# Performance work log

Hardware: AMD Instinct MI355X
Metric: run time of the kernel (lower is better)

The kernel has to match this reference:

```python
import jax, jax.numpy as jnp
import numpy as np

N = 50000       # nodes
E = 800000      # edges (before self loops)
F_IN = 256      # num_features
HID = 64        # hidden_dim
HEADS = 4       # num_heads
NEG = 0.2       # negative_slope
LN_EPS = 1e-5


def setup_inputs() -> dict:
    key = jax.random.key(0)
    ks = jax.random.split(key, 24)
    g = lambda k, shape, s=0.05: jax.random.normal(k, shape, jnp.float32) * s
    inp = {
        "x": jax.random.normal(ks[0], (N, F_IN), jnp.float32),
        "edge_index": jax.random.randint(ks[1], (2, E), 0, N, jnp.int32),
        # gat1: in=F_IN, out=HID per head, HEADS heads, concat=True
        "W1": g(ks[2], (HEADS * HID, F_IN)),
        "att_src1": g(ks[3], (HEADS, HID)),
        "att_dst1": g(ks[4], (HEADS, HID)),
        "b1": g(ks[5], (HEADS * HID,)),
        # gat2: in=HEADS*HID, out=HID, 1 head
        "W2": g(ks[6], (HID, HEADS * HID)),
        "att_src2": g(ks[7], (1, HID)),
        "att_dst2": g(ks[8], (1, HID)),
        "b2": g(ks[9], (HID,)),
        # lin_in residual projection
        "lin_w": g(ks[10], (HID, F_IN)),
        "lin_b": g(ks[11], (HID,)),
        # LayerNorm
        "gamma": jnp.ones((HID,), jnp.float32),
        "beta": jnp.zeros((HID,), jnp.float32),
        # GRU (1 layer, input=HID, hidden=HID), gate order r,z,n as in torch
        "w_ih": g(ks[12], (3 * HID, HID)),
        "w_hh": g(ks[13], (3 * HID, HID)),
        "b_ih": g(ks[14], (3 * HID,)),
        "b_hh": g(ks[15], (3 * HID,)),
        # fc head -> 3 classes
        "fc_w": g(ks[16], (3, HID)),
        "fc_b": g(ks[17], (3,)),
    }
    return inp


def gat_conv(x, W, att_src, att_dst, bias, src, dst, heads, n_nodes):
    """PyG-style GATConv (eval mode: no dropout). src/dst include self loops."""
    h = (x @ W.T).reshape(n_nodes, heads, -1)            # [N,H,C]
    a_src = jnp.einsum('nhc,hc->nh', h, att_src)          # [N,H]
    a_dst = jnp.einsum('nhc,hc->nh', h, att_dst)
    e = jax.nn.leaky_relu(a_src[src] + a_dst[dst], NEG)   # [E',H]
    m = jax.ops.segment_max(e, dst, num_segments=n_nodes) # scatter-softmax over dst
    e = jnp.exp(e - m[dst])
    s = jax.ops.segment_sum(e, dst, num_segments=n_nodes)
    alpha = e / s[dst]                                    # [E',H]
    out = jax.ops.segment_sum(alpha[:, :, None] * h[src], dst, num_segments=n_nodes)
    return out.reshape(n_nodes, -1) + bias                # concat heads + bias


def reference(x, edge_index, W1, att_src1, att_dst1, b1, W2, att_src2, att_dst2, b2,
              lin_w, lin_b, gamma, beta, w_ih, w_hh, b_ih, b_hh, fc_w, fc_b):
    n = x.shape[0]
    loops = jnp.arange(n, dtype=edge_index.dtype)
    src = jnp.concatenate([edge_index[0], loops])  # add_self_loops=True default
    dst = jnp.concatenate([edge_index[1], loops])

    h = jax.nn.leaky_relu(gat_conv(x, W1, att_src1, att_dst1, b1, src, dst, HEADS, n), NEG)
    # F.dropout is identity in eval mode
    h = gat_conv(h, W2, att_src2, att_dst2, b2, src, dst, 1, n)
    h = jax.nn.leaky_relu(h, NEG)
    # LayerNorm (torch uses biased variance)
    mu = h.mean(-1, keepdims=True)
    var = ((h - mu) ** 2).mean(-1, keepdims=True)
    h = (h - mu) / jnp.sqrt(var + LN_EPS) * gamma + beta
    h = h + x @ lin_w.T + lin_b
    # single-step GRU with h0 = 0 (seq_len == 1)
    gi = h @ w_ih.T + b_ih                 # [N,3C]
    i_r, i_z, i_n = jnp.split(gi, 3, axis=-1)
    h_r, h_z, h_n = jnp.split(b_hh, 3)     # W_hh @ 0 == 0
    r = jax.nn.sigmoid(i_r + h_r)
    z = jax.nn.sigmoid(i_z + h_z)
    ng = jnp.tanh(i_n + r * h_n)
    hy = (1.0 - z) * ng                    # + z * h_prev(=0)
    return hy @ fc_w.T + fc_b              # [N,3]
```

## Files before the change

### kernel.cpp

```cpp
#include <hip/hip_runtime.h>
#include <hip/hip_bf16.h>

#define N_NODES 50000
#define N_EDGES 800000
#define F_IN 256
#define HID 64
#define HEADS 4
#define NEG 0.2f
#define LN_EPS 1e-5f

typedef _Float16 half8 __attribute__((ext_vector_type(8)));
typedef _Float16 half4v __attribute__((ext_vector_type(4)));
typedef float floatx4 __attribute__((ext_vector_type(4)));

__device__ __forceinline__ float wave_sum(float v) {
    #pragma unroll
    for (int o = 32; o > 0; o >>= 1) v += __shfl_xor(v, o, 64);
    return v;
}
__device__ __forceinline__ int wave_sum_i(int v) {
    #pragma unroll
    for (int o = 32; o > 0; o >>= 1) v += __shfl_xor(v, o, 64);
    return v;
}
__device__ __forceinline__ float leaky(float x) { return x > 0.0f ? x : NEG * x; }

__global__ void count_kernel(const int* __restrict__ dst, int* __restrict__ deg,
                             int E, int Etot) {
    int e = blockIdx.x * blockDim.x + threadIdx.x;
    if (e >= Etot) return;
    int d = (e < E) ? dst[e] : (e - E);
    atomicAdd(&deg[d], 1);
}

__global__ void scan_part(const int* __restrict__ deg, int* __restrict__ bsum, int N) {
    int tid = threadIdx.x;
    int i = blockIdx.x * 256 + tid;
    int v = (i < N) ? deg[i] : 0;
    int s = wave_sum_i(v);
    __shared__ int ws4[4];
    if ((tid & 63) == 0) ws4[tid >> 6] = s;
    __syncthreads();
    if (tid == 0) bsum[blockIdx.x] = ws4[0] + ws4[1] + ws4[2] + ws4[3];
}

__global__ void scan_top(int* __restrict__ bsum, int nb) {
    __shared__ int sh[256];
    int t = threadIdx.x;
    int v = (t < nb) ? bsum[t] : 0;
    sh[t] = v;
    __syncthreads();
    for (int o = 1; o < 256; o <<= 1) {
        int u = (t >= o) ? sh[t - o] : 0;
        __syncthreads();
        sh[t] += u;
        __syncthreads();
    }
    if (t < nb) bsum[t] = sh[t] - v;
}

__global__ void scan_final(const int* __restrict__ deg, const int* __restrict__ bsum,
                           int* __restrict__ row_ptr, int N) {
    __shared__ int sh[256];
    int t = threadIdx.x;
    int i = blockIdx.x * 256 + t;
    int v = (i < N) ? deg[i] : 0;
    sh[t] = v;
    __syncthreads();
    for (int o = 1; o < 256; o <<= 1) {
        int u = (t >= o) ? sh[t - o] : 0;
        __syncthreads();
        sh[t] += u;
        __syncthreads();
    }
    if (i < N) row_ptr[i + 1] = bsum[blockIdx.x] + sh[t];
    if (i == 0) row_ptr[0] = 0;
}

__global__ void scatter_kernel(const int* __restrict__ src, const int* __restrict__ dst,
                               const int* __restrict__ row_ptr, int* __restrict__ fill,
                               int* __restrict__ col, int E, int Etot) {
    int e = blockIdx.x * blockDim.x + threadIdx.x;
    if (e >= Etot) return;
    int s, d;
    if (e < E) { s = src[e]; d = dst[e]; }
    else       { s = d = e - E; }
    int pos = atomicAdd(&fill[d], 1);
    col[row_ptr[d] + pos] = s;
}

struct CvtJob { const float* src; _Float16* dst; int len; };
__global__ void cvt_f16_multi(CvtJob j0, CvtJob j1, CvtJob j2, CvtJob j3, CvtJob j4) {
    int idx = (blockIdx.x * blockDim.x + threadIdx.x) * 4;
    const float* s; _Float16* d; int rel = idx;
    if      (rel < j0.len) { s = j0.src; d = j0.dst; }
    else if ((rel -= j0.len) < j1.len) { s = j1.src; d = j1.dst; }
    else if ((rel -= j1.len) < j2.len) { s = j2.src; d = j2.dst; }
    else if ((rel -= j2.len) < j3.len) { s = j3.src; d = j3.dst; }
    else if ((rel -= j3.len) < j4.len) { s = j4.src; d = j4.dst; }
    else return;
    float4 v = *(const float4*)(s + rel);
    half4v h;
    h[0] = (_Float16)v.x; h[1] = (_Float16)v.y;
    h[2] = (_Float16)v.z; h[3] = (_Float16)v.w;
    *(half4v*)(d + rel) = h;
}

template<int NT, int H, typename OutT>
__global__ __launch_bounds__(256, 2)
void gemm_mfma(const _Float16* __restrict__ A, const _Float16* __restrict__ B,
               const float* __restrict__ bias, OutT* __restrict__ Cout,
               const float* __restrict__ att_s, const float* __restrict__ att_d,
               float* __restrict__ a_srcO, float* __restrict__ a_dstO,
               int M, int K, int add_bias) {
    constexpr int Nc = NT * 16;
    constexpr int BROW = 40;
    constexpr int BTILE = Nc * BROW * 2;
    constexpr int TILEB = 16 * Nc * sizeof(OutT);
    constexpr int SM = (BTILE > 4 * TILEB) ? BTILE : 4 * TILEB;
    __shared__ __align__(16) char smem[SM];
    _Float16* sB = (_Float16*)smem;
    int tid = threadIdx.x;
    int w = tid >> 6, lane = tid & 63;
    int m_base = blockIdx.x * 64 + w * 16;
    bool active = (m_base < M);
    int r = lane & 15, q = lane >> 4;
    const _Float16* ap = A + (size_t)(m_base + r) * K + q * 8;
    floatx4 acc[NT];
    #pragma unroll
    for (int t = 0; t < NT; ++t) acc[t] = (floatx4){0.f, 0.f, 0.f, 0.f};
    half8 a_next = {};
    if (active) a_next = *(const half8*)ap;
    for (int k0 = 0; k0 < K; k0 += 32) {
        for (int i = tid; i < Nc * 4; i += 256) {
            int row = i >> 2, seg = i & 3;
            *(half8*)(sB + row * BROW + seg * 8) =
                *(const half8*)(B + (size_t)row * K + k0 + seg * 8);
        }
        __syncthreads();
        half8 a = a_next;
        if (active && k0 + 32 < K) a_next = *(const half8*)(ap + k0 + 32);
        if (active) {
            half8 b[NT];
            #pragma unroll
            for (int t = 0; t < NT; ++t)
                b[t] = *(const half8*)(sB + (t * 16 + r) * BROW + q * 8);
            #pragma unroll
            for (int t = 0; t < NT; ++t)
                acc[t] = __builtin_amdgcn_mfma_f32_16x16x32_f16(a, b[t], acc[t], 0, 0, 0);
        }
        __syncthreads();
    }
    if (active) {
        OutT* st = (OutT*)(smem + w * TILEB);
        #pragma unroll
        for (int t = 0; t < NT; ++t) {
            int cc = t * 16 + r;
            float bv = add_bias ? bias[cc] : 0.0f;
            #pragma unroll
            for (int rr = 0; rr < 4; ++rr)
                st[(q * 4 + rr) * Nc + cc] = (OutT)(acc[t][rr] + bv);
        }
        constexpr int NISS = TILEB / 1024;
        const int4* src = (const int4*)st;
        int4* dst = (int4*)((char*)Cout + (size_t)m_base * (Nc * sizeof(OutT)));
        #pragma unroll
        for (int i = 0; i < NISS; ++i) dst[i * 64 + lane] = src[i * 64 + lane];
        if constexpr (H > 0) {
            float ps[H][4], pd[H][4];
            #pragma unroll
            for (int h = 0; h < H; ++h) {
                #pragma unroll
                for (int rr = 0; rr < 4; ++rr) { ps[h][rr] = 0.f; pd[h][rr] = 0.f; }
                #pragma unroll
                for (int tt = 0; tt < 4; ++tt) {
                    int t = h * 4 + tt;
                    float as = att_s[t * 16 + r];
                    float ad = att_d[t * 16 + r];
                    #pragma unroll
                    for (int rr = 0; rr < 4; ++rr) {
                        ps[h][rr] += acc[t][rr] * as;
                        pd[h][rr] += acc[t][rr] * ad;
                    }
                }
            }
            #pragma unroll
            for (int m = 1; m < 16; m <<= 1) {
                #pragma unroll
                for (int h = 0; h < H; ++h)
                    #pragma unroll
                    for (int rr = 0; rr < 4; ++rr) {
                        ps[h][rr] += __shfl_xor(ps[h][rr], m, 64);
                        pd[h][rr] += __shfl_xor(pd[h][rr], m, 64);
                    }
            }
            if (r == 0) {
                #pragma unroll
                for (int rr = 0; rr < 4; ++rr) {
                    int gm = m_base + q * 4 + rr;
                    #pragma unroll
                    for (int h = 0; h < H; ++h) {
                        a_srcO[gm * H + h] = ps[h][rr];
                        a_dstO[gm * H + h] = pd[h][rr];
                    }
                }
            }
        }
    }
}

__global__ void gat_agg4(const _Float16* __restrict__ h, const float* __restrict__ a_src,
                         const float* __restrict__ a_dst, const int* __restrict__ row_ptr,
                         const int* __restrict__ col, const float* __restrict__ bias,
                         _Float16* __restrict__ outp, int N) {
    int w = threadIdx.x >> 6, lane = threadIdx.x & 63;
    int i = blockIdx.x * 4 + w;
    if (i >= N) return;
    __shared__ float alphS[4][256];
    __shared__ int   scolS[4][64];
    float* alph = alphS[w];
    int*   scol = scolS[w];
    int start = row_ptr[i], end = row_ptr[i + 1];
    int deg = end - start;
    float4 ad4 = *(const float4*)(a_dst + i * 4);

    if (deg <= 64) {
        float e0 = 0.f, e1 = 0.f, e2 = 0.f, e3 = 0.f; int s = 0;
        if (lane < deg) {
            s = col[start + lane];
            float4 as4 = *(const float4*)(a_src + (size_t)s * 4);
            e0 = __expf(leaky(as4.x + ad4.x));
            e1 = __expf(leaky(as4.y + ad4.y));
            e2 = __expf(leaky(as4.z + ad4.z));
            e3 = __expf(leaky(as4.w + ad4.w));
        }
        float s0 = wave_sum(e0), s1 = wave_sum(e1), s2 = wave_sum(e2), s3 = wave_sum(e3);
        float4 al = make_float4(0.f, 0.f, 0.f, 0.f);
        int so = 0;
        if (lane < deg) {
            al = make_float4(e0 / s0, e1 / s1, e2 / s2, e3 / s3);
            so = s << 9;
        }
        *(float4*)(alph + lane * 4) = al;
        scol[lane] = so;
        int half32 = lane >> 5;
        int fl = lane & 31;
        int flb = fl * 16;
        int ahofs = half32 * 4 + (fl >> 3);
        const char* hB = (const char*)h;
        float acc[8];
        #pragma unroll
        for (int k = 0; k < 8; ++k) acc[k] = 0.f;
        int dpad = (deg + 7) & ~7;
        for (int j = 0; j < dpad; j += 8) {
            int o0 = scol[j + half32];
            int o1 = scol[j + 2 + half32];
            int o2 = scol[j + 4 + half32];
            int o3 = scol[j + 6 + half32];
            half8 v0 = *(const half8*)(hB + (flb + o0));
            half8 v1 = *(const half8*)(hB + (flb + o1));
            half8 v2 = *(const half8*)(hB + (flb + o2));
            half8 v3 = *(const half8*)(hB + (flb + o3));
            float a0 = alph[j * 4 + ahofs];
            float a1 = alph[j * 4 + 8 + ahofs];
            float a2 = alph[j * 4 + 16 + ahofs];
            float a3 = alph[j * 4 + 24 + ahofs];
            #pragma unroll
            for (int k = 0; k < 8; ++k) acc[k] += a0 * (float)v0[k];
            #pragma unroll
            for (int k = 0; k < 8; ++k) acc[k] += a1 * (float)v1[k];
            #pragma unroll
            for (int k = 0; k < 8; ++k) acc[k] += a2 * (float)v2[k];
            #pragma unroll
            for (int k = 0; k < 8; ++k) acc[k] += a3 * (float)v3[k];
        }
        #pragma unroll
        for (int k = 0; k < 8; ++k) acc[k] += __shfl_xor(acc[k], 32, 64);
        if (lane < 32) {
            half8 o8;
            #pragma unroll
            for (int k = 0; k < 8; ++k)
                o8[k] = (_Float16)leaky(acc[k] + bias[fl * 8 + k]);
            *(half8*)(outp + (size_t)i * 256 + fl * 8) = o8;
        }
    } else {
        int hh = lane >> 4;
        const _Float16* hb = h + lane * 4;
        float4 acc = make_float4(0.f, 0.f, 0.f, 0.f);
        float t0 = 0.f, t1 = 0.f, t2 = 0.f, t3 = 0.f;
        for (int j = start + lane; j < end; j += 64) {
            int s = col[j];
            float4 as4 = *(const float4*)(a_src + (size_t)s * 4);
            t0 += __expf(leaky(as4.x + ad4.x));
            t1 += __expf(leaky(as4.y + ad4.y));
            t2 += __expf(leaky(as4.z + ad4.z));
            t3 += __expf(leaky(as4.w + ad4.w));
        }
        t0 = wave_sum(t0); t1 = wave_sum(t1); t2 = wave_sum(t2); t3 = wave_sum(t3);
        float adh = (hh == 0) ? ad4.x : (hh == 1) ? ad4.y : (hh == 2) ? ad4.z : ad4.w;
        float ih  = 1.0f / ((hh == 0) ? t0 : (hh == 1) ? t1 : (hh == 2) ? t2 : t3);
        for (int j = start; j < end; ++j) {
            int s = col[j];
            float asv = a_src[(size_t)s * 4 + hh];
            float alpha = __expf(leaky(asv + adh)) * ih;
            half4v v = *(const half4v*)(hb + (size_t)s * 256);
            acc.x += alpha * (float)v[0]; acc.y += alpha * (float)v[1];
            acc.z += alpha * (float)v[2]; acc.w += alpha * (float)v[3];
        }
        float4 bv = *(const float4*)(bias + lane * 4);
        half4v o;
        o[0] = (_Float16)leaky(acc.x + bv.x);
        o[1] = (_Float16)leaky(acc.y + bv.y);
        o[2] = (_Float16)leaky(acc.z + bv.z);
        o[3] = (_Float16)leaky(acc.w + bv.w);
        *(half4v*)(outp + (size_t)i * 256 + lane * 4) = o;
    }
}

__global__ void gat_agg1_ln(const _Float16* __restrict__ h, const float* __restrict__ a_src,
                            const float* __restrict__ a_dst, const int* __restrict__ row_ptr,
                            const int* __restrict__ col, const float* __restrict__ bias,
                            const float* __restrict__ lin, const float* __restrict__ gamma,
                            const float* __restrict__ beta, _Float16* __restrict__ hresh,
                            int N) {
    int w = threadIdx.x >> 6, lane = threadIdx.x & 63;
    int i = blockIdx.x * 4 + w;
    if (i >= N) return;
    __shared__ float alphS[4][64];
    __shared__ int   scolS[4][64];
    float* alph = alphS[w];
    int*   scol = scolS[w];
    int start = row_ptr[i], end = row_ptr[i + 1];
    int deg = end - start;
    float ad = a_dst[i];
    int sub = lane >> 4;
    int c4 = (lane & 15) * 4;
    float4 acc = make_float4(0.f, 0.f, 0.f, 0.f);

    if (deg <= 64) {
        float e = 0.f; int s = 0;
        if (lane < deg) {
            s = col[start + lane];
            e = __expf(leaky(a_src[s] + ad));
        }
        float ss = wave_sum(e);
        if (lane < deg) { alph[lane] = e / ss; scol[lane] = s; }
        int j = sub;
        for (; j + 4 < deg; j += 8) {
            int s0 = scol[j], s1 = scol[j + 4];
            float a0 = alph[j], a1 = alph[j + 4];
            half4v v0 = *(const half4v*)(h + (size_t)s0 * 64 + c4);
            half4v v1 = *(const half4v*)(h + (size_t)s1 * 64 + c4);
            acc.x += a0 * (float)v0[0] + a1 * (float)v1[0];
            acc.y += a0 * (float)v0[1] + a1 * (float)v1[1];
            acc.z += a0 * (float)v0[2] + a1 * (float)v1[2];
            acc.w += a0 * (float)v0[3] + a1 * (float)v1[3];
        }
        for (; j < deg; j += 4) {
            int s = scol[j];
            float a0 = alph[j];
            half4v v = *(const half4v*)(h + (size_t)s * 64 + c4);
            acc.x += a0 * (float)v[0]; acc.y += a0 * (float)v[1];
            acc.z += a0 * (float)v[2]; acc.w += a0 * (float)v[3];
        }
    } else {
        float ssum = 0.f;
        for (int j = start + lane; j < end; j += 64)
            ssum += __expf(leaky(a_src[col[j]] + ad));
        ssum = wave_sum(ssum);
        float inv = 1.0f / ssum;
        for (int j = start + sub; j < end; j += 4) {
            int s = col[j];
            float alpha = __expf(leaky(a_src[s] + ad)) * inv;
            half4v v = *(const half4v*)(h + (size_t)s * 64 + c4);
            acc.x += alpha * (float)v[0]; acc.y += alpha * (float)v[1];
            acc.z += alpha * (float)v[2]; acc.w += alpha * (float)v[3];
        }
    }
    #pragma unroll
    for (int o = 16; o <= 32; o <<= 1) {
        acc.x += __shfl_xor(acc.x, o, 64);
        acc.y += __shfl_xor(acc.y, o, 64);
        acc.z += __shfl_xor(acc.z, o, 64);
        acc.w += __shfl_xor(acc.w, o, 64);
    }
    float4 bv = *(const float4*)(bias + c4);
    float o0 = leaky(acc.x + bv.x), o1 = leaky(acc.y + bv.y);
    float o2 = leaky(acc.z + bv.z), o3 = leaky(acc.w + bv.w);
    float ls = o0 + o1 + o2 + o3;
    #pragma unroll
    for (int o = 1; o <= 8; o <<= 1) ls += __shfl_xor(ls, o, 64);
    float mu = ls * (1.0f / 64.0f);
    float d0 = o0 - mu, d1 = o1 - mu, d2 = o2 - mu, d3 = o3 - mu;
    float lq = d0 * d0 + d1 * d1 + d2 * d2 + d3 * d3;
    #pragma unroll
    for (int o = 1; o <= 8; o <<= 1) lq += __shfl_xor(lq, o, 64);
    float rstd = rsqrtf(lq * (1.0f / 64.0f) + LN_EPS);
    float4 g4 = *(const float4*)(gamma + c4);
    float4 b4 = *(const float4*)(beta + c4);
    float4 l4 = *(const float4*)(lin + (size_t)i * 64 + c4);
    if (sub == 0) {
        half4v hv;
        hv[0] = (_Float16)(d0 * rstd * g4.x + b4.x + l4.x);
        hv[1] = (_Float16)(d1 * rstd * g4.y + b4.y + l4.y);
        hv[2] = (_Float16)(d2 * rstd * g4.z + b4.z + l4.z);
        hv[3] = (_Float16)(d3 * rstd * g4.w + b4.w + l4.w);
        *(half4v*)(hresh + (size_t)i * 64 + c4) = hv;
    }
}

__global__ __launch_bounds__(256, 2)
void gemm_gru(const _Float16* __restrict__ A, const _Float16* __restrict__ B,
              const float* __restrict__ b_ih, const float* __restrict__ b_hh,
              const float* __restrict__ fc_w, const float* __restrict__ fc_b,
              float* __restrict__ outp, int M) {
    const int K = 64, NT = 12, Nc = 192;
    constexpr int BROW = 40;
    __shared__ __align__(16) char smem[4 * 16 * 192 * 2];
    _Float16* sB = (_Float16*)smem;
    int tid = threadIdx.x;
    int w = tid >> 6, lane = tid & 63;
    int m_base = blockIdx.x * 64 + w * 16;
    bool active = (m_base < M);
    int r = lane & 15, q = lane >> 4;
    const _Float16* ap = A + (size_t)(m_base + r) * K + q * 8;
    floatx4 acc[NT];
    #pragma unroll
    for (int t = 0; t < NT; ++t) acc[t] = (floatx4){0.f, 0.f, 0.f, 0.f};
    half8 a_next = {};
    if (active) a_next = *(const half8*)ap;
    for (int k0 = 0; k0 < K; k0 += 32) {
        for (int i = tid; i < Nc * 4; i += 256) {
            int row = i >> 2, seg = i & 3;
            *(half8*)(sB + row * BROW + seg * 8) =
                *(const half8*)(B + (size_t)row * K + k0 + seg * 8);
        }
        __syncthreads();
        half8 a = a_next;
        if (active && k0 + 32 < K) a_next = *(const half8*)(ap + k0 + 32);
        if (active) {
            half8 b[NT];
            #pragma unroll
            for (int t = 0; t < NT; ++t)
                b[t] = *(const half8*)(sB + (t * 16 + r) * BROW + q * 8);
            #pragma unroll
            for (int t = 0; t < NT; ++t)
                acc[t] = __builtin_amdgcn_mfma_f32_16x16x32_f16(a, b[t], acc[t], 0, 0, 0);
        }
        __syncthreads();
    }
    if (!active) return;
    _Float16* sw = (_Float16*)smem + w * 16 * 192;
    #pragma unroll
    for (int t = 0; t < NT; ++t) {
        int cc = t * 16 + r;
        float bv = b_ih[cc];
        #pragma unroll
        for (int rr = 0; rr < 4; ++rr)
            sw[(q * 4 + rr) * Nc + cc] = (_Float16)(acc[t][rr] + bv);
    }
    float br_[4], bz_[4], bn_[4], f0_[4], f1_[4], f2_[4];
    *(float4*)br_ = *(const float4*)(b_hh + r * 4);
    *(float4*)bz_ = *(const float4*)(b_hh + 64 + r * 4);
    *(float4*)bn_ = *(const float4*)(b_hh + 128 + r * 4);
    *(float4*)f0_ = *(const float4*)(fc_w + r * 4);
    *(float4*)f1_ = *(const float4*)(fc_w + 64 + r * 4);
    *(float4*)f2_ = *(const float4*)(fc_w + 128 + r * 4);
    #pragma unroll
    for (int rr = 0; rr < 4; ++rr) {
        int row = q * 4 + rr;
        const _Float16* g = sw + row * Nc;
        half4v ir4 = *(const half4v*)(g + r * 4);
        half4v iz4 = *(const half4v*)(g + 64 + r * 4);
        half4v in4 = *(const half4v*)(g + 128 + r * 4);
        float p0 = 0.f, p1 = 0.f, p2 = 0.f;
        #pragma unroll
        for (int k = 0; k < 4; ++k) {
            float rg = 1.0f / (1.0f + __expf(-((float)ir4[k] + br_[k])));
            float zg = 1.0f / (1.0f + __expf(-((float)iz4[k] + bz_[k])));
            float ng = tanhf((float)in4[k] + rg * bn_[k]);
            float hy = (1.0f - zg) * ng;
            p0 += hy * f0_[k]; p1 += hy * f1_[k]; p2 += hy * f2_[k];
        }
        #pragma unroll
        for (int o = 1; o <= 8; o <<= 1) {
            p0 += __shfl_xor(p0, o, 64);
            p1 += __shfl_xor(p1, o, 64);
            p2 += __shfl_xor(p2, o, 64);
        }
        if (r == 0) {
            int gm = m_base + row;
            outp[(size_t)gm * 3 + 0] = p0 + fc_b[0];
            outp[(size_t)gm * 3 + 1] = p1 + fc_b[1];
            outp[(size_t)gm * 3 + 2] = p2 + fc_b[2];
        }
    }
}

extern "C" void kernel_launch(void* const* d_in, const int* in_sizes, int n_in,
                              void* d_out, int out_size, void* d_ws, size_t ws_size,
                              hipStream_t stream) {
    const float* x        = (const float*)d_in[0];
    const int*   ei       = (const int*)d_in[1];
    const float* W1       = (const float*)d_in[2];
    const float* att_src1 = (const float*)d_in[3];
    const float* att_dst1 = (const float*)d_in[4];
    const float* b1       = (const float*)d_in[5];
    const float* W2       = (const float*)d_in[6];
    const float* att_src2 = (const float*)d_in[7];
    const float* att_dst2 = (const float*)d_in[8];
    const float* b2       = (const float*)d_in[9];
    const float* lin_w    = (const float*)d_in[10];
    const float* lin_b    = (const float*)d_in[11];
    const float* gamma    = (const float*)d_in[12];
    const float* beta     = (const float*)d_in[13];
    const float* w_ih     = (const float*)d_in[14];
    const float* b_ih     = (const float*)d_in[16];
    const float* b_hh     = (const float*)d_in[17];
    const float* fc_w     = (const float*)d_in[18];
    const float* fc_b     = (const float*)d_in[19];
    float* out = (float*)d_out;

    const int N = N_NODES, E = N_EDGES;
    const int Etot = E + N;
    const int nb = (N + 255) / 256;
    char* ws = (char*)d_ws;

    size_t off = 0;
    auto alloc = [&](size_t bytes) {
        size_t o = off;
        off = (off + bytes + 255) & ~(size_t)255;
        return o;
    };
    int*      row_ptr = (int*)(ws + alloc((size_t)(N + 1) * 4));
    int*      col     = (int*)(ws + alloc((size_t)Etot * 4));
    int*      deg     = (int*)(ws + alloc((size_t)N * 4));
    int*      fill    = (int*)(ws + alloc((size_t)N * 4));
    int*      bsum    = (int*)(ws + alloc((size_t)nb * 4));
    float*    a_src1b = (float*)(ws + alloc((size_t)N * HEADS * 4));
    float*    a_dst1b = (float*)(ws + alloc((size_t)N * HEADS * 4));
    float*    a_src2b = (float*)(ws + alloc((size_t)N * 4));
    float*    a_dst2b = (float*)(ws + alloc((size_t)N * 4));
    _Float16* W1h     = (_Float16*)(ws + alloc((size_t)256 * 256 * 2));
    _Float16* W2h     = (_Float16*)(ws + alloc((size_t)64 * 256 * 2));
    _Float16* lin_wh  = (_Float16*)(ws + alloc((size_t)64 * 256 * 2));
    _Float16* w_ihh   = (_Float16*)(ws + alloc((size_t)192 * 64 * 2));
    char* big = ws + alloc((size_t)64000000);
    _Float16* xh   = (_Float16*)big;
    _Float16* h1h  = (_Float16*)(big + 25600000);
    float*    lin  = (float*)(big + 51200000);
    char* r3 = ws + alloc((size_t)25600000);
    _Float16* o1h   = (_Float16*)r3;
    _Float16* hresh = (_Float16*)r3;
    char* r4 = ws + alloc((size_t)6400000);
    _Float16* h2h = (_Float16*)r4;

    hipMemsetAsync(deg, 0, (size_t)N * 4, stream);
    hipMemsetAsync(fill, 0, (size_t)N * 4, stream);

    count_kernel<<<(Etot + 255) / 256, 256, 0, stream>>>(ei + E, deg, E, Etot);
    scan_part<<<nb, 256, 0, stream>>>(deg, bsum, N);
    scan_top<<<1, 256, 0, stream>>>(bsum, nb);
    scan_final<<<nb, 256, 0, stream>>>(deg, bsum, row_ptr, N);
    scatter_kernel<<<(Etot + 255) / 256, 256, 0, stream>>>(ei, ei + E, row_ptr, fill, col, E, Etot);

    {
        CvtJob j0{x, xh, N * F_IN};
        CvtJob j1{W1, W1h, 256 * 256};
        CvtJob j2{W2, W2h, 64 * 256};
        CvtJob j3{lin_w, lin_wh, 64 * 256};
        CvtJob j4{w_ih, w_ihh, 192 * 64};
        int total4 = (j0.len + j1.len + j2.len + j3.len + j4.len) / 4;
        cvt_f16_multi<<<(total4 + 255) / 256, 256, 0, stream>>>(j0, j1, j2, j3, j4);
    }

    const int gmBlocks = (N + 63) / 64;
    const int aggBlocks = (N + 3) / 4;

    gemm_mfma<16, 4, _Float16><<<gmBlocks, 256, 0, stream>>>(xh, W1h, nullptr, h1h,
        att_src1, att_dst1, a_src1b, a_dst1b, N, 256, 0);
    gat_agg4<<<aggBlocks, 256, 0, stream>>>(h1h, a_src1b, a_dst1b, row_ptr, col, b1, o1h, N);

    gemm_mfma<4, 0, float><<<gmBlocks, 256, 0, stream>>>(xh, lin_wh, lin_b, lin,
        nullptr, nullptr, nullptr, nullptr, N, 256, 1);

    gemm_mfma<4, 1, _Float16><<<gmBlocks, 256, 0, stream>>>(o1h, W2h, nullptr, h2h,
        att_src2, att_dst2, a_src2b, a_dst2b, N, 256, 0);

    gat_agg1_ln<<<aggBlocks, 256, 0, stream>>>(h2h, a_src2b, a_dst2b, row_ptr, col, b2,
        lin, gamma, beta, hresh, N);

    gemm_gru<<<gmBlocks, 256, 0, stream>>>(hresh, w_ihh, b_ih, b_hh, fc_w, fc_b, out, N);
}
```

Baseline: 371.8 us.

## Fuse lin_in projection into layer-1 GEMM and use packed fp16 FMA in aggregation

The residual lin_in projection is merged into the first GAT GEMM by concatenating its weights after W1, giving a 320-column fp16 output whose last 64 columns hold the residual. This removes a separate GEMM launch and its second read of x, and the residual is now stored in fp16 instead of fp32. The layer-1 aggregation also switches to packed half2 FMAs with fp16 attention weights, partially accumulating in fp16 before adding into fp32. The cost is a wider row stride (640 bytes) for gathers, and some precision loss from fp16 alpha, fp16 partial sums and the fp16 residual.

```diff
diff --git a/kernel.cpp b/kernel.cpp
--- a/kernel.cpp
+++ b/kernel.cpp
@@ -11,7 +11,11 @@
 
 typedef _Float16 half8 __attribute__((ext_vector_type(8)));
 typedef _Float16 half4v __attribute__((ext_vector_type(4)));
+typedef _Float16 half2v __attribute__((ext_vector_type(2)));
 typedef float floatx4 __attribute__((ext_vector_type(4)));
+
+union H2U { unsigned u; half2v h; };
+union H8U { half8 v; half2v h2[4]; };
 
 __device__ __forceinline__ float wave_sum(float v) {
     #pragma unroll
@@ -112,7 +116,7 @@
                const float* __restrict__ bias, OutT* __restrict__ Cout,
                const float* __restrict__ att_s, const float* __restrict__ att_d,
                float* __restrict__ a_srcO, float* __restrict__ a_dstO,
-               int M, int K, int add_bias) {
+               int M, int K, int bias_mode) {
     constexpr int Nc = NT * 16;
     constexpr int BROW = 40;
     constexpr int BTILE = Nc * BROW * 2;
@@ -156,7 +160,9 @@
         #pragma unroll
         for (int t = 0; t < NT; ++t) {
             int cc = t * 16 + r;
-            float bv = add_bias ? bias[cc] : 0.0f;
+            float bv = 0.f;
+            if (bias_mode == 1) bv = bias[cc];
+            else if (bias_mode == 2 && cc >= 256) bv = bias[cc - 256];
             #pragma unroll
             for (int rr = 0; rr < 4; ++rr)
                 st[(q * 4 + rr) * Nc + cc] = (OutT)(acc[t][rr] + bv);
@@ -216,10 +222,10 @@
     int w = threadIdx.x >> 6, lane = threadIdx.x & 63;
     int i = blockIdx.x * 4 + w;
     if (i >= N) return;
-    __shared__ float alphS[4][256];
-    __shared__ int   scolS[4][64];
-    float* alph = alphS[w];
-    int*   scol = scolS[w];
+    __shared__ unsigned alphS[4][256];
+    __shared__ int      scolS[4][64];
+    unsigned* alph = alphS[w];
+    int*      scol = scolS[w];
     int start = row_ptr[i], end = row_ptr[i + 1];
     int deg = end - start;
     float4 ad4 = *(const float4*)(a_dst + i * 4);
@@ -239,9 +245,14 @@
         int so = 0;
         if (lane < deg) {
             al = make_float4(e0 / s0, e1 / s1, e2 / s2, e3 / s3);
-            so = s << 9;
-        }
-        *(float4*)(alph + lane * 4) = al;
+            so = s * 640;
+        }
+        H2U p0, p1, p2, p3;
+        _Float16 t0 = (_Float16)al.x; p0.h = (half2v){t0, t0};
+        _Float16 t1 = (_Float16)al.y; p1.h = (half2v){t1, t1};
+        _Float16 t2 = (_Float16)al.z; p2.h = (half2v){t2, t2};
+        _Float16 t3 = (_Float16)al.w; p3.h = (half2v){t3, t3};
+        *(uint4*)(alph + lane * 4) = make_uint4(p0.u, p1.u, p2.u, p3.u);
         scol[lane] = so;
         int half32 = lane >> 5;
         int fl = lane & 31;
@@ -257,22 +268,25 @@
             int o1 = scol[j + 2 + half32];
             int o2 = scol[j + 4 + half32];
             int o3 = scol[j + 6 + half32];
-            half8 v0 = *(const half8*)(hB + (flb + o0));
-            half8 v1 = *(const half8*)(hB + (flb + o1));
-            half8 v2 = *(const half8*)(hB + (flb + o2));
-            half8 v3 = *(const half8*)(hB + (flb + o3));
-            float a0 = alph[j * 4 + ahofs];
-            float a1 = alph[j * 4 + 8 + ahofs];
-            float a2 = alph[j * 4 + 16 + ahofs];
-            float a3 = alph[j * 4 + 24 + ahofs];
-            #pragma unroll
-            for (int k = 0; k < 8; ++k) acc[k] += a0 * (float)v0[k];
-            #pragma unroll
-            for (int k = 0; k < 8; ++k) acc[k] += a1 * (float)v1[k];
-            #pragma unroll
-            for (int k = 0; k < 8; ++k) acc[k] += a2 * (float)v2[k];
-            #pragma unroll
-            for (int k = 0; k < 8; ++k) acc[k] += a3 * (float)v3[k];
+            H8U v0, v1, v2, v3;
+            v0.v = *(const half8*)(hB + (flb + o0));
+            v1.v = *(const half8*)(hB + (flb + o1));
+            v2.v = *(const half8*)(hB + (flb + o2));
+            v3.v = *(const half8*)(hB + (flb + o3));
+            H2U a0, a1, a2, a3;
+            a0.u = alph[j * 4 + ahofs];
+            a1.u = alph[j * 4 + 8 + ahofs];
+            a2.u = alph[j * 4 + 16 + ahofs];
+            a3.u = alph[j * 4 + 24 + ahofs];
+            #pragma unroll
+            for (int p = 0; p < 4; ++p) {
+                half2v hp = a0.h * v0.h2[p];
+                hp = __builtin_elementwise_fma(a1.h, v1.h2[p], hp);
+                hp = __builtin_elementwise_fma(a2.h, v2.h2[p], hp);
+                hp = __builtin_elementwise_fma(a3.h, v3.h2[p], hp);
+                acc[p * 2]     += (float)hp[0];
+                acc[p * 2 + 1] += (float)hp[1];
+            }
         }
         #pragma unroll
         for (int k = 0; k < 8; ++k) acc[k] += __shfl_xor(acc[k], 32, 64);
@@ -303,7 +317,7 @@
             int s = col[j];
             float asv = a_src[(size_t)s * 4 + hh];
             float alpha = __expf(leaky(asv + adh)) * ih;
-            half4v v = *(const half4v*)(hb + (size_t)s * 256);
+            half4v v = *(const half4v*)(hb + (size_t)s * 320);
             acc.x += alpha * (float)v[0]; acc.y += alpha * (float)v[1];
             acc.z += alpha * (float)v[2]; acc.w += alpha * (float)v[3];
         }
@@ -320,7 +334,7 @@
 __global__ void gat_agg1_ln(const _Float16* __restrict__ h, const float* __restrict__ a_src,
                             const float* __restrict__ a_dst, const int* __restrict__ row_ptr,
                             const int* __restrict__ col, const float* __restrict__ bias,
-                            const float* __restrict__ lin, const float* __restrict__ gamma,
+                            const _Float16* __restrict__ linh, const float* __restrict__ gamma,
                             const float* __restrict__ beta, _Float16* __restrict__ hresh,
                             int N) {
     int w = threadIdx.x >> 6, lane = threadIdx.x & 63;
@@ -398,13 +412,13 @@
     float rstd = rsqrtf(lq * (1.0f / 64.0f) + LN_EPS);
     float4 g4 = *(const float4*)(gamma + c4);
     float4 b4 = *(const float4*)(beta + c4);
-    float4 l4 = *(const float4*)(lin + (size_t)i * 64 + c4);
+    half4v l4 = *(const half4v*)(linh + (size_t)i * 320 + c4);
     if (sub == 0) {
         half4v hv;
-        hv[0] = (_Float16)(d0 * rstd * g4.x + b4.x + l4.x);
-        hv[1] = (_Float16)(d1 * rstd * g4.y + b4.y + l4.y);
-        hv[2] = (_Float16)(d2 * rstd * g4.z + b4.z + l4.z);
-        hv[3] = (_Float16)(d3 * rstd * g4.w + b4.w + l4.w);
+        hv[0] = (_Float16)(d0 * rstd * g4.x + b4.x + (float)l4[0]);
+        hv[1] = (_Float16)(d1 * rstd * g4.y + b4.y + (float)l4[1]);
+        hv[2] = (_Float16)(d2 * rstd * g4.z + b4.z + (float)l4[2]);
+        hv[3] = (_Float16)(d3 * rstd * g4.w + b4.w + (float)l4[3]);
         *(half4v*)(hresh + (size_t)i * 64 + c4) = hv;
     }
 }
@@ -541,14 +555,14 @@
     float*    a_dst1b = (float*)(ws + alloc((size_t)N * HEADS * 4));
     float*    a_src2b = (float*)(ws + alloc((size_t)N * 4));
     float*    a_dst2b = (float*)(ws + alloc((size_t)N * 4));
-    _Float16* W1h     = (_Float16*)(ws + alloc((size_t)256 * 256 * 2));
+    _Float16* B1big   = (_Float16*)(ws + alloc((size_t)320 * 256 * 2));
+    _Float16* W1h     = B1big;
+    _Float16* lin_wh  = B1big + 256 * 256;
     _Float16* W2h     = (_Float16*)(ws + alloc((size_t)64 * 256 * 2));
-    _Float16* lin_wh  = (_Float16*)(ws + alloc((size_t)64 * 256 * 2));
     _Float16* w_ihh   = (_Float16*)(ws + alloc((size_t)192 * 64 * 2));
     char* big = ws + alloc((size_t)64000000);
     _Float16* xh   = (_Float16*)big;
-    _Float16* h1h  = (_Float16*)(big + 25600000);
-    float*    lin  = (float*)(big + 51200000);
+    _Float16* h1L  = (_Float16*)(big + 25600000);
     char* r3 = ws + alloc((size_t)25600000);
     _Float16* o1h   = (_Float16*)r3;
     _Float16* hresh = (_Float16*)r3;
@@ -577,18 +591,15 @@
     const int gmBlocks = (N + 63) / 64;
     const int aggBlocks = (N + 3) / 4;
 
-    gemm_mfma<16, 4, _Float16><<<gmBlocks, 256, 0, stream>>>(xh, W1h, nullptr, h1h,
-        att_src1, att_dst1, a_src1b, a_dst1b, N, 256, 0);
-    gat_agg4<<<aggBlocks, 256, 0, stream>>>(h1h, a_src1b, a_dst1b, row_ptr, col, b1, o1h, N);
-
-    gemm_mfma<4, 0, float><<<gmBlocks, 256, 0, stream>>>(xh, lin_wh, lin_b, lin,
-        nullptr, nullptr, nullptr, nullptr, N, 256, 1);
+    gemm_mfma<20, 4, _Float16><<<gmBlocks, 256, 0, stream>>>(xh, B1big, lin_b, h1L,
+        att_src1, att_dst1, a_src1b, a_dst1b, N, 256, 2);
+    gat_agg4<<<aggBlocks, 256, 0, stream>>>(h1L, a_src1b, a_dst1b, row_ptr, col, b1, o1h, N);
 
     gemm_mfma<4, 1, _Float16><<<gmBlocks, 256, 0, stream>>>(o1h, W2h, nullptr, h2h,
         att_src2, att_dst2, a_src2b, a_dst2b, N, 256, 0);
 
     gat_agg1_ln<<<aggBlocks, 256, 0, stream>>>(h2h, a_src2b, a_dst2b, row_ptr, col, b2,
-        lin, gamma, beta, hresh, N);
+        h1L + 256, gamma, beta, hresh, N);
 
     gemm_gru<<<gmBlocks, 256, 0, stream>>>(hresh, w_ihh, b_ih, b_hh, fc_w, fc_b, out, N);
 }
```

New measurement: 362.3 us. 1.03x faster.
